# Performance work log

Measured on AMD Instinct MI355X. Metric: run time of the kernel, lower is better.

Reference implementation:

```python
import jax, jax.numpy as jnp
import numpy as np

B, T, C = 1, 2048, 4096
H, HS, NE = 32, 128, 32  # n_head, head_size, rope_n_elem


def setup_inputs() -> dict:
    key = jax.random.key(0)
    ks = jax.random.split(key, 7)
    sd = 1.0 / np.sqrt(C)
    return {
        "x": jax.random.normal(ks[0], (B, T, C), jnp.float32),
        "cos": jax.random.uniform(ks[1], (T, NE), jnp.float32, -1.0, 1.0),
        "sin": jax.random.uniform(ks[2], (T, NE), jnp.float32, -1.0, 1.0),
        "W_attn": jax.random.normal(ks[3], (3 * C, C), jnp.float32) * sd,
        "b_attn": jax.random.normal(ks[4], (3 * C,), jnp.float32) * 0.01,
        "W_proj": jax.random.normal(ks[5], (C, C), jnp.float32) * sd,
        "b_proj": jax.random.normal(ks[6], (C,), jnp.float32) * 0.01,
    }


def _apply_rope(t, cos, sin):
    # t: (B,H,T,HS); rope only on first NE dims
    tr, tp = t[..., :NE], t[..., NE:]
    x1, x2 = tr[..., : NE // 2], tr[..., NE // 2 :]
    rotated = jnp.concatenate([-x2, x1], axis=-1)
    c = cos[None, :, :]  # (1,T,NE) broadcasts over (B,H,T,NE)
    s = sin[None, :, :]
    return jnp.concatenate([tr * c + rotated * s, tp], axis=-1)


def reference(x, cos, sin, W_attn, b_attn, W_proj, b_proj):
    b, t, c = x.shape
    qkv = x @ W_attn.T + b_attn  # (B,T,3C)
    # view (B,T,G,total_qkv,HS) then permute -> (B,G,total_qkv,T,HS); G=H, q_per_kv=1
    qkv = qkv.reshape(b, t, H, 3, HS).transpose(0, 2, 3, 1, 4)
    q, k, v = qkv[:, :, 0], qkv[:, :, 1], qkv[:, :, 2]  # each (B,H,T,HS)
    q = _apply_rope(q, cos, sin)
    k = _apply_rope(k, cos, sin)
    scale = 1.0 / jnp.sqrt(jnp.asarray(HS, x.dtype))
    scores = jnp.einsum("bhqd,bhkd->bhqk", q, k) * scale
    causal = jnp.tril(jnp.ones((t, t), bool))
    scores = jnp.where(causal, scores, -jnp.inf)
    attn = jax.nn.softmax(scores, axis=-1)
    y = jnp.einsum("bhqk,bhkd->bhqd", attn, v)
    y = y.transpose(0, 2, 1, 3).reshape(b, t, H * HS)
    return y @ W_proj.T + b_proj
```

## Files before the change

kernel.cpp:

```cpp
#include <hip/hip_runtime.h>
#include <cstdint>
#include <cstddef>

typedef __bf16 bf16x8 __attribute__((ext_vector_type(8)));
typedef __bf16 bf16x4 __attribute__((ext_vector_type(4)));
typedef float fx4 __attribute__((ext_vector_type(4)));

static constexpr int T = 2048;
static constexpr int C = 4096;
static constexpr int H = 32;
static constexpr int HS = 128;
static constexpr int QKV_N = 12288;

#define MFMA16(a, b, c) __builtin_amdgcn_mfma_f32_16x16x32_bf16((a), (b), (c), 0, 0, 0)

__global__ __launch_bounds__(256) void cvt_f32_to_bf16(const float* __restrict__ in,
                                                       __bf16* __restrict__ out, int n4) {
  int i = blockIdx.x * 256 + threadIdx.x;
  if (i >= n4) return;
  float4 v = ((const float4*)in)[i];
  bf16x4 o;
  o.x = (__bf16)v.x; o.y = (__bf16)v.y; o.z = (__bf16)v.z; o.w = (__bf16)v.w;
  ((bf16x4*)out)[i] = o;
}

template <int OUT_BF16>
__global__ __launch_bounds__(256, 2) void gemm_bt(const __bf16* __restrict__ A,
                                                  const __bf16* __restrict__ B,
                                                  const float* __restrict__ bias,
                                                  void* __restrict__ Cout,
                                                  int M, int N, int K) {
  constexpr int BM = 128, BN = 128, BK = 64, LDT = BK + 8;
  __shared__ __align__(16) __bf16 As[BM * LDT];
  __shared__ __align__(16) __bf16 Bs[BN * LDT];
  const int tid = threadIdx.x;
  const int lane = tid & 63;
  const int wid = tid >> 6;
  const int wm = (wid >> 1) * 64;
  const int wn = (wid & 1) * 64;
  const int m0 = blockIdx.y * BM;
  const int n0 = blockIdx.x * BN;
  const int lr = lane & 15;
  const int quad = lane >> 4;

  fx4 acc[4][4] = {};

  for (int k0 = 0; k0 < K; k0 += BK) {
#pragma unroll
    for (int c = 0; c < 4; ++c) {
      int i = tid + c * 256;
      int r = i >> 3;
      int kp = (i & 7) * 8;
      *(uint4*)(&As[r * LDT + kp]) = *(const uint4*)(A + (size_t)(m0 + r) * K + k0 + kp);
      *(uint4*)(&Bs[r * LDT + kp]) = *(const uint4*)(B + (size_t)(n0 + r) * K + k0 + kp);
    }
    __syncthreads();
#pragma unroll
    for (int ks = 0; ks < BK; ks += 32) {
      bf16x8 af[4], bfr[4];
#pragma unroll
      for (int mm = 0; mm < 4; ++mm)
        af[mm] = *(const bf16x8*)(&As[(wm + mm * 16 + lr) * LDT + ks + quad * 8]);
#pragma unroll
      for (int nn = 0; nn < 4; ++nn)
        bfr[nn] = *(const bf16x8*)(&Bs[(wn + nn * 16 + lr) * LDT + ks + quad * 8]);
#pragma unroll
      for (int mm = 0; mm < 4; ++mm)
#pragma unroll
        for (int nn = 0; nn < 4; ++nn)
          acc[mm][nn] = MFMA16(af[mm], bfr[nn], acc[mm][nn]);
    }
    __syncthreads();
  }

#pragma unroll
  for (int nn = 0; nn < 4; ++nn) {
    int col = n0 + wn + nn * 16 + lr;
    float bv = bias[col];
#pragma unroll
    for (int mm = 0; mm < 4; ++mm) {
#pragma unroll
      for (int r = 0; r < 4; ++r) {
        int row = m0 + wm + mm * 16 + quad * 4 + r;
        float v = acc[mm][nn][r] + bv;
        if (OUT_BF16)
          ((__bf16*)Cout)[(size_t)row * N + col] = (__bf16)v;
        else
          ((float*)Cout)[(size_t)row * N + col] = v;
      }
    }
  }
}

__global__ __launch_bounds__(256) void rope_kernel(__bf16* __restrict__ qkv,
                                                   const float* __restrict__ cosp,
                                                   const float* __restrict__ sinp) {
  int tid = blockIdx.x * 256 + threadIdx.x;
  int d = tid & 15;
  int which = (tid >> 4) & 1;
  int h = (tid >> 5) & 31;
  int t = tid >> 10;
  size_t base = (size_t)t * QKV_N + h * 384 + which * 128;
  float x1 = (float)qkv[base + d];
  float x2 = (float)qkv[base + d + 16];
  float c1 = cosp[t * 32 + d], s1 = sinp[t * 32 + d];
  float c2 = cosp[t * 32 + d + 16], s2 = sinp[t * 32 + d + 16];
  qkv[base + d] = (__bf16)(x1 * c1 - x2 * s1);
  qkv[base + d + 16] = (__bf16)(x2 * c2 + x1 * s2);
}

__global__ __launch_bounds__(256) void vtrans_kernel(const __bf16* __restrict__ qkv,
                                                     __bf16* __restrict__ vt) {
  __shared__ __align__(16) __bf16 tile[64][136];
  int h = blockIdx.x;
  int t0 = blockIdx.y * 64;
  int tid = threadIdx.x;
#pragma unroll
  for (int c = 0; c < 4; ++c) {
    int i = tid + c * 256;
    int tl = i >> 4;
    int dp = (i & 15) * 8;
    *(uint4*)(&tile[tl][dp]) = *(const uint4*)(qkv + (size_t)(t0 + tl) * QKV_N + h * 384 + 256 + dp);
  }
  __syncthreads();
#pragma unroll
  for (int c = 0; c < 32; ++c) {
    int o = tid + c * 256;
    int d = o >> 6;
    int tl = o & 63;
    vt[((size_t)h * 128 + d) * T + t0 + tl] = tile[tl][d];
  }
}

__global__ __launch_bounds__(256, 2) void attn_kernel(const __bf16* __restrict__ qkv,
                                                      const __bf16* __restrict__ vt,
                                                      __bf16* __restrict__ y) {
  constexpr int KT = 64;
  constexpr int LKS = HS + 8;
  constexpr int LVS = KT + 8;
  constexpr int LPS = KT + 8;
  __shared__ __align__(16) __bf16 Ks[KT * LKS];
  __shared__ __align__(16) __bf16 Vs[HS * LVS];
  __shared__ __align__(16) __bf16 Ps[4][16 * LPS];

  const int h = blockIdx.x;
  const int qb = blockIdx.y;
  const int q0 = qb * 64;
  const int tid = threadIdx.x;
  const int lane = tid & 63;
  const int wid = tid >> 6;
  const int lr = lane & 15;
  const int quad = lane >> 4;
  const int qrow = q0 + wid * 16;

  bf16x8 qf[4];
#pragma unroll
  for (int kk = 0; kk < 4; ++kk)
    qf[kk] = *(const bf16x8*)(qkv + (size_t)(qrow + lr) * QKV_N + h * 384 + kk * 32 + quad * 8);

  float m_i[4], l_i[4];
  fx4 acc_o[8];
#pragma unroll
  for (int r = 0; r < 4; ++r) { m_i[r] = -1e30f; l_i[r] = 0.f; }
#pragma unroll
  for (int dd = 0; dd < 8; ++dd) acc_o[dd] = (fx4)0.f;

  const float scale = 0.08838834764831845f;
  const int ntiles = qb + 1;
  for (int kt = 0; kt < ntiles; ++kt) {
    const int kbase = kt * KT;
#pragma unroll
    for (int c = 0; c < 4; ++c) {
      int i = tid + c * 256;
      int r = i >> 4;
      int dp = (i & 15) * 8;
      *(uint4*)(&Ks[r * LKS + dp]) =
          *(const uint4*)(qkv + (size_t)(kbase + r) * QKV_N + h * 384 + 128 + dp);
    }
#pragma unroll
    for (int c = 0; c < 4; ++c) {
      int i = tid + c * 256;
      int r = i >> 3;
      int kp = (i & 7) * 8;
      *(uint4*)(&Vs[r * LVS + kp]) =
          *(const uint4*)(vt + ((size_t)h * 128 + r) * T + kbase + kp);
    }
    __syncthreads();

    fx4 sv[4] = {};
#pragma unroll
    for (int nn = 0; nn < 4; ++nn) {
#pragma unroll
      for (int kk = 0; kk < 4; ++kk) {
        bf16x8 kf = *(const bf16x8*)(&Ks[(nn * 16 + lr) * LKS + kk * 32 + quad * 8]);
        sv[nn] = MFMA16(qf[kk], kf, sv[nn]);
      }
    }

    float rmax[4], rsum[4];
#pragma unroll
    for (int r = 0; r < 4; ++r) rmax[r] = -1e30f;
#pragma unroll
    for (int nn = 0; nn < 4; ++nn) {
      int kj = kbase + nn * 16 + lr;
#pragma unroll
      for (int r = 0; r < 4; ++r) {
        int qi = qrow + quad * 4 + r;
        float v = sv[nn][r] * scale;
        v = (kj > qi) ? -1e30f : v;
        sv[nn][r] = v;
        rmax[r] = fmaxf(rmax[r], v);
      }
    }
#pragma unroll
    for (int off = 1; off < 16; off <<= 1)
#pragma unroll
      for (int r = 0; r < 4; ++r)
        rmax[r] = fmaxf(rmax[r], __shfl_xor(rmax[r], off, 64));

    float alpha[4];
#pragma unroll
    for (int r = 0; r < 4; ++r) {
      float mnew = fmaxf(m_i[r], rmax[r]);
      alpha[r] = __expf(m_i[r] - mnew);
      m_i[r] = mnew;
      rsum[r] = 0.f;
    }
#pragma unroll
    for (int nn = 0; nn < 4; ++nn) {
#pragma unroll
      for (int r = 0; r < 4; ++r) {
        float p = __expf(sv[nn][r] - m_i[r]);
        sv[nn][r] = p;
        rsum[r] += p;
      }
    }
#pragma unroll
    for (int off = 1; off < 16; off <<= 1)
#pragma unroll
      for (int r = 0; r < 4; ++r)
        rsum[r] += __shfl_xor(rsum[r], off, 64);
#pragma unroll
    for (int r = 0; r < 4; ++r)
      l_i[r] = l_i[r] * alpha[r] + rsum[r];
#pragma unroll
    for (int dd = 0; dd < 8; ++dd)
#pragma unroll
      for (int r = 0; r < 4; ++r)
        acc_o[dd][r] *= alpha[r];

#pragma unroll
    for (int nn = 0; nn < 4; ++nn)
#pragma unroll
      for (int r = 0; r < 4; ++r)
        Ps[wid][(quad * 4 + r) * LPS + nn * 16 + lr] = (__bf16)sv[nn][r];
    asm volatile("s_waitcnt lgkmcnt(0)" ::: "memory");

#pragma unroll
    for (int kc = 0; kc < 2; ++kc) {
      bf16x8 pf = *(const bf16x8*)(&Ps[wid][lr * LPS + kc * 32 + quad * 8]);
#pragma unroll
      for (int dd = 0; dd < 8; ++dd) {
        bf16x8 vf = *(const bf16x8*)(&Vs[(dd * 16 + lr) * LVS + kc * 32 + quad * 8]);
        acc_o[dd] = MFMA16(pf, vf, acc_o[dd]);
      }
    }
    __syncthreads();
  }

#pragma unroll
  for (int r = 0; r < 4; ++r) l_i[r] = 1.0f / l_i[r];
#pragma unroll
  for (int dd = 0; dd < 8; ++dd)
#pragma unroll
    for (int r = 0; r < 4; ++r) {
      int row = qrow + quad * 4 + r;
      int col = h * 128 + dd * 16 + lr;
      y[(size_t)row * C + col] = (__bf16)(acc_o[dd][r] * l_i[r]);
    }
}

extern "C" void kernel_launch(void* const* d_in, const int* in_sizes, int n_in,
                              void* d_out, int out_size, void* d_ws, size_t ws_size,
                              hipStream_t stream) {
  const float* x      = (const float*)d_in[0];
  const float* cosp   = (const float*)d_in[1];
  const float* sinp   = (const float*)d_in[2];
  const float* W_attn = (const float*)d_in[3];
  const float* b_attn = (const float*)d_in[4];
  const float* W_proj = (const float*)d_in[5];
  const float* b_proj = (const float*)d_in[6];
  float* out = (float*)d_out;

  char* wsb = (char*)d_ws;
  __bf16* Wab  = (__bf16*)(wsb + 0);
  __bf16* Wpb  = (__bf16*)(wsb + 100663296);
  __bf16* xb   = (__bf16*)(wsb + 134217728);
  __bf16* qkvb = (__bf16*)(wsb + 150994944);
  __bf16* yb   = (__bf16*)(wsb + 201326592);
  __bf16* vtb  = (__bf16*)(wsb + 218103808);

  cvt_f32_to_bf16<<<8192, 256, 0, stream>>>(x, xb, (T * C) / 4);
  cvt_f32_to_bf16<<<49152, 256, 0, stream>>>(W_attn, Wab, (QKV_N * C) / 4);
  cvt_f32_to_bf16<<<16384, 256, 0, stream>>>(W_proj, Wpb, (C * C) / 4);

  gemm_bt<1><<<dim3(96, 16), 256, 0, stream>>>(xb, Wab, b_attn, (void*)qkvb, T, QKV_N, C);

  rope_kernel<<<8192, 256, 0, stream>>>(qkvb, cosp, sinp);
  vtrans_kernel<<<dim3(32, 32), 256, 0, stream>>>(qkvb, vtb);

  attn_kernel<<<dim3(32, 32), 256, 0, stream>>>(qkvb, vtb, yb);

  gemm_bt<0><<<dim3(32, 16), 256, 0, stream>>>(yb, Wpb, b_proj, (void*)out, T, C, C);
}
```

Baseline: 847.2 us.

## Load GEMM and attention tiles directly into LDS via global_load_lds

Replaces the register-staged global-to-shared tile copies in the GEMM and attention kernels with 16-byte `global_load_lds` copies. Each wave fills a contiguous 1 KB chunk, which forces the shared tiles to drop their row padding. The goal is to save VGPRs and the extra register round trip during tile loads. The unpadded 128-byte row stride risks LDS bank conflicts on the MFMA fragment reads. The V-transpose kernel also now gathers 8 elements per thread and writes them as one 16-byte vector store instead of scalar stores.

```diff
diff --git a/kernel.cpp b/kernel.cpp
--- a/kernel.cpp
+++ b/kernel.cpp
@@ -13,6 +13,12 @@
 static constexpr int QKV_N = 12288;
 
 #define MFMA16(a, b, c) __builtin_amdgcn_mfma_f32_16x16x32_bf16((a), (b), (c), 0, 0, 0)
+
+__device__ __forceinline__ void async_cp16(const void* g, void* l) {
+  __builtin_amdgcn_global_load_lds((const __attribute__((address_space(1))) unsigned int*)g,
+                                   (__attribute__((address_space(3))) unsigned int*)l,
+                                   16, 0, 0);
+}
 
 __global__ __launch_bounds__(256) void cvt_f32_to_bf16(const float* __restrict__ in,
                                                        __bf16* __restrict__ out, int n4) {
@@ -30,9 +36,9 @@
                                                   const float* __restrict__ bias,
                                                   void* __restrict__ Cout,
                                                   int M, int N, int K) {
-  constexpr int BM = 128, BN = 128, BK = 64, LDT = BK + 8;
-  __shared__ __align__(16) __bf16 As[BM * LDT];
-  __shared__ __align__(16) __bf16 Bs[BN * LDT];
+  constexpr int BM = 128, BN = 128, BK = 64;
+  __shared__ __align__(16) __bf16 As[BM * BK];
+  __shared__ __align__(16) __bf16 Bs[BN * BK];
   const int tid = threadIdx.x;
   const int lane = tid & 63;
   const int wid = tid >> 6;
@@ -48,11 +54,12 @@
   for (int k0 = 0; k0 < K; k0 += BK) {
 #pragma unroll
     for (int c = 0; c < 4; ++c) {
-      int i = tid + c * 256;
-      int r = i >> 3;
-      int kp = (i & 7) * 8;
-      *(uint4*)(&As[r * LDT + kp]) = *(const uint4*)(A + (size_t)(m0 + r) * K + k0 + kp);
-      *(uint4*)(&Bs[r * LDT + kp]) = *(const uint4*)(B + (size_t)(n0 + r) * K + k0 + kp);
+      int chunk = wid * 4 + c;
+      int e8 = chunk * 64 + lane;
+      int r = e8 >> 3;
+      int kp = (e8 & 7) * 8;
+      async_cp16(A + (size_t)(m0 + r) * K + k0 + kp, &As[chunk * 512]);
+      async_cp16(B + (size_t)(n0 + r) * K + k0 + kp, &Bs[chunk * 512]);
     }
     __syncthreads();
 #pragma unroll
@@ -60,10 +67,10 @@
       bf16x8 af[4], bfr[4];
 #pragma unroll
       for (int mm = 0; mm < 4; ++mm)
-        af[mm] = *(const bf16x8*)(&As[(wm + mm * 16 + lr) * LDT + ks + quad * 8]);
+        af[mm] = *(const bf16x8*)(&As[(wm + mm * 16 + lr) * BK + ks + quad * 8]);
 #pragma unroll
       for (int nn = 0; nn < 4; ++nn)
-        bfr[nn] = *(const bf16x8*)(&Bs[(wn + nn * 16 + lr) * LDT + ks + quad * 8]);
+        bfr[nn] = *(const bf16x8*)(&Bs[(wn + nn * 16 + lr) * BK + ks + quad * 8]);
 #pragma unroll
       for (int mm = 0; mm < 4; ++mm)
 #pragma unroll
@@ -124,11 +131,14 @@
   }
   __syncthreads();
 #pragma unroll
-  for (int c = 0; c < 32; ++c) {
+  for (int c = 0; c < 4; ++c) {
     int o = tid + c * 256;
-    int d = o >> 6;
-    int tl = o & 63;
-    vt[((size_t)h * 128 + d) * T + t0 + tl] = tile[tl][d];
+    int d = o >> 3;
+    int ts = (o & 7) * 8;
+    bf16x8 v;
+#pragma unroll
+    for (int j = 0; j < 8; ++j) v[j] = tile[ts + j][d];
+    *(bf16x8*)(vt + ((size_t)h * 128 + d) * T + t0 + ts) = v;
   }
 }
 
@@ -136,11 +146,9 @@
                                                       const __bf16* __restrict__ vt,
                                                       __bf16* __restrict__ y) {
   constexpr int KT = 64;
-  constexpr int LKS = HS + 8;
-  constexpr int LVS = KT + 8;
   constexpr int LPS = KT + 8;
-  __shared__ __align__(16) __bf16 Ks[KT * LKS];
-  __shared__ __align__(16) __bf16 Vs[HS * LVS];
+  __shared__ __align__(16) __bf16 Ks[KT * HS];
+  __shared__ __align__(16) __bf16 Vs[HS * KT];
   __shared__ __align__(16) __bf16 Ps[4][16 * LPS];
 
   const int h = blockIdx.x;
@@ -171,19 +179,19 @@
     const int kbase = kt * KT;
 #pragma unroll
     for (int c = 0; c < 4; ++c) {
-      int i = tid + c * 256;
-      int r = i >> 4;
-      int dp = (i & 15) * 8;
-      *(uint4*)(&Ks[r * LKS + dp]) =
-          *(const uint4*)(qkv + (size_t)(kbase + r) * QKV_N + h * 384 + 128 + dp);
+      int chunk = wid * 4 + c;
+      int e8 = chunk * 64 + lane;
+      int r = e8 >> 4;
+      int dp = (e8 & 15) * 8;
+      async_cp16(qkv + (size_t)(kbase + r) * QKV_N + h * 384 + 128 + dp, &Ks[chunk * 512]);
     }
 #pragma unroll
     for (int c = 0; c < 4; ++c) {
-      int i = tid + c * 256;
-      int r = i >> 3;
-      int kp = (i & 7) * 8;
-      *(uint4*)(&Vs[r * LVS + kp]) =
-          *(const uint4*)(vt + ((size_t)h * 128 + r) * T + kbase + kp);
+      int chunk = wid * 4 + c;
+      int e8 = chunk * 64 + lane;
+      int r = e8 >> 3;
+      int kp = (e8 & 7) * 8;
+      async_cp16(vt + ((size_t)h * 128 + r) * T + kbase + kp, &Vs[chunk * 512]);
     }
     __syncthreads();
 
@@ -192,7 +200,7 @@
     for (int nn = 0; nn < 4; ++nn) {
 #pragma unroll
       for (int kk = 0; kk < 4; ++kk) {
-        bf16x8 kf = *(const bf16x8*)(&Ks[(nn * 16 + lr) * LKS + kk * 32 + quad * 8]);
+        bf16x8 kf = *(const bf16x8*)(&Ks[(nn * 16 + lr) * HS + kk * 32 + quad * 8]);
         sv[nn] = MFMA16(qf[kk], kf, sv[nn]);
       }
     }
@@ -261,7 +269,7 @@
       bf16x8 pf = *(const bf16x8*)(&Ps[wid][lr * LPS + kc * 32 + quad * 8]);
 #pragma unroll
       for (int dd = 0; dd < 8; ++dd) {
-        bf16x8 vf = *(const bf16x8*)(&Vs[(dd * 16 + lr) * LVS + kc * 32 + quad * 8]);
+        bf16x8 vf = *(const bf16x8*)(&Vs[(dd * 16 + lr) * KT + kc * 32 + quad * 8]);
         acc_o[dd] = MFMA16(pf, vf, acc_o[dd]);
       }
     }
```

Result: slower. 912.1 us (+7.7%).
